# Kernel tuning notes

Hardware: AMD Instinct MI355X
Metric: run time of the kernel (lower is better)

## Reference

```python
import jax, jax.numpy as jnp
import numpy as np

P = 2        # patch_size
HEADS = 1


def _conv(x, w, b, groups=1):
    # NCHW conv, kernel 3x3, SAME padding (stride 1)
    y = jax.lax.conv_general_dilated(
        x, w, window_strides=(1, 1), padding='SAME',
        dimension_numbers=('NCHW', 'OIHW', 'NCHW'),
        feature_group_count=groups)
    return y + b[None, :, None, None]


def _unfold(x, p):
    # torch.nn.Unfold(kernel=p, stride=p): [B,C,h,w] -> [B, C*p*p, n]
    B, C, h, w = x.shape
    x = x.reshape(B, C, h // p, p, w // p, p)
    x = x.transpose(0, 1, 3, 5, 2, 4)  # (B, C, ph, pw, h/p, w/p)
    return x.reshape(B, C * p * p, (h // p) * (w // p))


def _fold(x, p, h, w):
    # inverse of _unfold (non-overlapping patches)
    B = x.shape[0]
    C = x.shape[1] // (p * p)
    x = x.reshape(B, C, p, p, h // p, w // p)
    x = x.transpose(0, 1, 4, 2, 5, 3)  # (B, C, h/p, ph, w/p, pw)
    return x.reshape(B, C, h, w)


def setup_inputs() -> dict:
    key = jax.random.key(0)
    ks = jax.random.split(key, 9)
    c = 64
    x = jax.random.normal(ks[0], (2, 5, c, 64, 64), jnp.float32)
    wq = jax.random.normal(ks[1], (c, 1, 3, 3), jnp.float32) * 0.1
    bq = jax.random.normal(ks[2], (c,), jnp.float32) * 0.1
    wk = jax.random.normal(ks[3], (c, 1, 3, 3), jnp.float32) * 0.1
    bk = jax.random.normal(ks[4], (c,), jnp.float32) * 0.1
    wv = jax.random.normal(ks[5], (c, c, 3, 3), jnp.float32) * 0.05
    bv = jax.random.normal(ks[6], (c,), jnp.float32) * 0.1
    wc = jax.random.normal(ks[7], (c, c, 3, 3), jnp.float32) * 0.05
    bc = jax.random.normal(ks[8], (c,), jnp.float32) * 0.1
    return {"x": x, "wq": wq, "bq": bq, "wk": wk, "bk": bk,
            "wv": wv, "bv": bv, "wc": wc, "bc": bc}


def reference(x, wq, bq, wk, bk, wv, bv, wc, bc):
    b, t, c, h, w = x.shape
    p, H = P, HEADS
    D = p * p * c           # 256
    d = D // H              # per-head dim
    n = (h // p) * (w // p)  # tokens per frame

    xf = x.reshape(b * t, c, h, w)
    q = _conv(xf, wq, bq, groups=c)   # depthwise
    k = _conv(xf, wk, bk, groups=c)   # depthwise
    v = _conv(xf, wv, bv)             # dense conv

    def to_tokens(y):
        # [bt, D, n] -> [b, H, d, t*n]
        u = _unfold(y, p).reshape(b, t, H, d, n)
        return u.transpose(0, 2, 3, 1, 4).reshape(b, H, d, t * n)

    uq, uk, uv = to_tokens(q), to_tokens(k), to_tokens(v)

    attn = jnp.einsum('bhdi,bhdj->bhij', uq, uk) * (d ** -0.5)
    attn = jax.nn.softmax(attn, axis=-1)           # [b,H,tn,tn]
    ax = jnp.einsum('bhij,bhdj->bhid', attn, uv)   # [b,H,tn,d]

    ax = ax.reshape(b, H, t, n, d).transpose(0, 2, 1, 4, 3).reshape(b * t, D, n)
    feat = _fold(ax, p, h, w)                      # [bt, c, h, w]
    out = _conv(feat, wc, bc).reshape(x.shape) + x
    return out
```

## Files before the change

kernel.cpp:

```cpp
#include <hip/hip_runtime.h>
#include <hip/hip_bf16.h>

typedef __attribute__((ext_vector_type(8))) short short8;
typedef __attribute__((ext_vector_type(8))) unsigned short ushort8;
typedef __attribute__((ext_vector_type(4))) unsigned short ushort4v;
typedef __attribute__((ext_vector_type(4))) float f32x4;

#define NTOK 5120
#define DDIM 256

__device__ __forceinline__ unsigned short f2bf(float f) {
  union { float f; unsigned int u; } x; x.f = f;
  unsigned int r = x.u + 0x7FFFu + ((x.u >> 16) & 1u);
  return (unsigned short)(r >> 16);
}

__global__ __launch_bounds__(256) void qk_gen(
    const float* __restrict__ xin, const float* __restrict__ wq,
    const float* __restrict__ bq, const float* __restrict__ wk,
    const float* __restrict__ bk, unsigned short* __restrict__ qt,
    unsigned short* __restrict__ kt)
{
  const int ch = blockIdx.x;
  const int bt = blockIdx.y;
  const int b = bt / 5, tf = bt % 5;
  const int tid = threadIdx.x;
  const float* xp = xin + ((size_t)bt * 64 + ch) * 4096;
  float wqv[9], wkv[9];
  #pragma unroll
  for (int i = 0; i < 9; i++) { wqv[i] = wq[ch * 9 + i]; wkv[i] = wk[ch * 9 + i]; }
  const float bqv = bq[ch], bkv = bk[ch];

  #pragma unroll
  for (int p = 0; p < 4; p++) {
    int pid = tid + p * 256;
    int gy = pid >> 5, gx = pid & 31;
    float v[4][4];
    #pragma unroll
    for (int r = 0; r < 4; r++) {
      int yy = 2 * gy - 1 + r;
      #pragma unroll
      for (int cc = 0; cc < 4; cc++) {
        int xx = 2 * gx - 1 + cc;
        bool ok = (yy >= 0) && (yy < 64) && (xx >= 0) && (xx < 64);
        v[r][cc] = ok ? xp[yy * 64 + xx] : 0.f;
      }
    }
    unsigned short qo[4], ko[4];
    #pragma unroll
    for (int py = 0; py < 2; py++)
      #pragma unroll
      for (int px = 0; px < 2; px++) {
        float aq = bqv, ak = bkv;
        #pragma unroll
        for (int dy = 0; dy < 3; dy++)
          #pragma unroll
          for (int dx = 0; dx < 3; dx++) {
            float xv = v[py + dy][px + dx];
            aq += wqv[dy * 3 + dx] * xv;
            ak += wkv[dy * 3 + dx] * xv;
          }
        qo[py * 2 + px] = f2bf(aq);
        ko[py * 2 + px] = f2bf(ak);
      }
    size_t base = ((size_t)(b * NTOK + tf * 1024 + pid)) * DDIM + ch * 4;
    ushort4v qv = { qo[0], qo[1], qo[2], qo[3] };
    ushort4v kv = { ko[0], ko[1], ko[2], ko[3] };
    *(ushort4v*)(qt + base) = qv;
    *(ushort4v*)(kt + base) = kv;
  }
}

__global__ __launch_bounds__(256) void wt_gen(
    const float* __restrict__ w0, const float* __restrict__ w1,
    unsigned short* __restrict__ o0, unsigned short* __restrict__ o1)
{
  const int tap = blockIdx.x;
  const float* src = blockIdx.y ? w1 : w0;
  unsigned short* dst = blockIdx.y ? o1 : o0;
  const int t = threadIdx.x;
  #pragma unroll
  for (int i = 0; i < 16; i++) {
    int oi = t + i * 256;
    dst[tap * 4096 + oi] = f2bf(src[(size_t)oi * 9 + tap]);
  }
}

__global__ __launch_bounds__(256) void conv_mfma(
    const float* __restrict__ src,
    const unsigned short* __restrict__ wt,
    float* __restrict__ dst)
{
  const int strip = blockIdx.x;
  const int bt = blockIdx.y;
  const int y0 = strip * 4;
  const int tid = threadIdx.x;
  const int sw = tid >> 6, lane = tid & 63;
  const int g = lane >> 4, c = lane & 15;

  __shared__ __align__(16) unsigned short lds_in[6 * 66 * 64];
  __shared__ __align__(16) unsigned short lds_w[64 * 64];

  {
    const int rr0 = lane >> 4;
    const int cb = lane & 15;
    #pragma unroll
    for (int pass = 0; pass < 2; ++pass) {
      int rr = pass * 4 + rr0;
      if (rr < 6) {
        int row = y0 - 1 + rr;
        bool rok = (row >= 0) && (row < 64);
        #pragma unroll 4
        for (int cii = 0; cii < 16; ++cii) {
          int ci = sw * 16 + cii;
          f32x4 v = { 0.f, 0.f, 0.f, 0.f };
          if (rok) v = *(const f32x4*)(src + ((size_t)(bt * 64 + ci)) * 4096 + row * 64 + cb * 4);
          char* base = (char*)lds_in + (rr * 66) * 128 + (ci & 7) * 2;
          #pragma unroll
          for (int q = 0; q < 4; ++q) {
            int lcol = cb * 4 + q + 1;
            *(unsigned short*)(base + lcol * 128 + (((ci >> 3) ^ (lcol & 7)) * 16)) = f2bf(v[q]);
          }
          if (cb == 0)
            *(unsigned short*)(base + (((ci >> 3) ^ 0) * 16)) = 0;
          if (cb == 15)
            *(unsigned short*)(base + 65 * 128 + (((ci >> 3) ^ 1) * 16)) = 0;
        }
      }
    }
  }

  f32x4 acc[4][4];
  #pragma unroll
  for (int ct = 0; ct < 4; ct++)
    #pragma unroll
    for (int xt = 0; xt < 4; xt++) acc[ct][xt] = (f32x4){ 0.f, 0.f, 0.f, 0.f };

  #pragma unroll 1
  for (int tap = 0; tap < 9; ++tap) {
    __syncthreads();
    {
      const unsigned short* wp = wt + tap * 4096;
      #pragma unroll
      for (int h = 0; h < 2; ++h) {
        int el = h * 2048 + tid * 8;
        int co = el >> 6, sl = (el & 63) >> 3;
        short8 wv8 = *(const short8*)(wp + el);
        *(short8*)((char*)lds_w + co * 128 + ((sl ^ (co & 7)) * 16)) = wv8;
      }
    }
    __syncthreads();
    const int dy = tap / 3 - 1, dx = tap % 3 - 1;
    const int rowp = sw + 1 + dy;
    #pragma unroll
    for (int kblk = 0; kblk < 2; ++kblk) {
      short8 af[4], bf[4];
      #pragma unroll
      for (int ct = 0; ct < 4; ++ct)
        af[ct] = *(const short8*)((char*)lds_w + (ct * 16 + c) * 128 + ((((kblk << 2) + g) ^ (c & 7)) * 16));
      #pragma unroll
      for (int xt = 0; xt < 4; ++xt) {
        int lcol = xt * 16 + c + dx + 1;
        bf[xt] = *(const short8*)((char*)lds_in + (rowp * 66 + lcol) * 128 + ((((kblk << 2) + g) ^ (lcol & 7)) * 16));
      }
      #pragma unroll
      for (int ct = 0; ct < 4; ++ct)
        #pragma unroll
        for (int xt = 0; xt < 4; ++xt)
          acc[ct][xt] = __builtin_amdgcn_mfma_f32_16x16x32_bf16(af[ct], bf[xt], acc[ct][xt], 0, 0, 0);
    }
  }

  const int y = y0 + sw;
  float* dp = dst + ((size_t)bt * 64) * 4096 + y * 64;
  #pragma unroll
  for (int ct = 0; ct < 4; ++ct)
    #pragma unroll
    for (int xt = 0; xt < 4; ++xt)
      #pragma unroll
      for (int r = 0; r < 4; ++r) {
        int co = ct * 16 + g * 4 + r;
        dp[(size_t)co * 4096 + xt * 16 + c] = acc[ct][xt][r];
      }
}

__global__ __launch_bounds__(256) void v_combine(
    const float* __restrict__ part, const float* __restrict__ bv,
    unsigned short* __restrict__ vt)
{
  const int co = blockIdx.x;
  const int bt = blockIdx.y;
  const int b = bt / 5, tf = bt % 5;
  const int t = threadIdx.x;
  const int y = t >> 2, xq = (t & 3) * 16;
  const float vb = bv[co];
  const float* p0 = part + ((size_t)bt * 64 + co) * 4096 + y * 64 + xq;
  float val[16];
  #pragma unroll
  for (int q = 0; q < 4; q++) {
    f32x4 a = *(const f32x4*)(p0 + q * 4);
    val[q*4+0] = a[0] + vb; val[q*4+1] = a[1] + vb;
    val[q*4+2] = a[2] + vb; val[q*4+3] = a[3] + vb;
  }
  int py = y & 1, gy = y >> 1;
  ushort8 w0, w1;
  #pragma unroll
  for (int i = 0; i < 8; i++) {
    w0[i] = f2bf(val[2 * i + 0]);
    w1[i] = f2bf(val[2 * i + 1]);
  }
  size_t base0 = ((size_t)(b * DDIM + co * 4 + py * 2)) * NTOK + tf * 1024 + gy * 32 + (xq >> 1);
  *(ushort8*)(vt + base0) = w0;
  *(ushort8*)(vt + base0 + NTOK) = w1;
}

__global__ __launch_bounds__(256) void attn_kernel(
    const unsigned short* __restrict__ qt, const unsigned short* __restrict__ kt,
    const unsigned short* __restrict__ vt, float* __restrict__ po,
    float* __restrict__ pm, float* __restrict__ pl, int jchunk)
{
  const int b = blockIdx.z;
  const int jc = blockIdx.y;
  const int njc = gridDim.y;
  const int i0 = blockIdx.x * 128;
  const int tid = threadIdx.x;
  const int w = tid >> 6, lane = tid & 63;
  const int g = lane >> 4, c = lane & 15;

  __shared__ __align__(16) unsigned short lds_k[64 * 256];
  __shared__ __align__(16) unsigned short lds_v[256 * 64];
  __shared__ __align__(16) unsigned short lds_p[4 * 32 * 64];

  short8 qf[2][8];
  #pragma unroll
  for (int st = 0; st < 2; st++) {
    const unsigned short* qr = qt + ((size_t)(b * NTOK + i0 + w * 32 + st * 16 + c)) * DDIM + g * 8;
    #pragma unroll
    for (int kb = 0; kb < 8; kb++) qf[st][kb] = *(const short8*)(qr + kb * 32);
  }
  f32x4 o[32];
  #pragma unroll
  for (int i = 0; i < 32; i++) o[i] = (f32x4){ 0.f, 0.f, 0.f, 0.f };
  float m[2][4], l[2][4];
  #pragma unroll
  for (int st = 0; st < 2; st++)
    #pragma unroll
    for (int r = 0; r < 4; r++) { m[st][r] = -1e30f; l[st][r] = 0.f; }

  const int sr = tid >> 5, sc = tid & 31;
  const int vdr = tid >> 3, vcc = tid & 7;

  const int jbeg = jc * jchunk;
  for (int j0 = jbeg; j0 < jbeg + jchunk; j0 += 64) {
    #pragma unroll
    for (int p = 0; p < 8; p++) {
      int row = sr + p * 8;
      short8 kv = *(const short8*)(kt + ((size_t)(b * NTOK + j0 + row)) * DDIM + sc * 8);
      *(short8*)((char*)lds_k + row * 512 + ((sc ^ (row & 7)) * 16)) = kv;
    }
    #pragma unroll
    for (int p = 0; p < 8; p++) {
      int dd = vdr + p * 32;
      short8 vv = *(const short8*)(vt + ((size_t)(b * DDIM + dd)) * NTOK + j0 + vcc * 8);
      *(short8*)((char*)lds_v + dd * 128 + ((vcc ^ (dd & 7)) * 16)) = vv;
    }
    __syncthreads();

    f32x4 s0[4], s1[4];
    #pragma unroll
    for (int js = 0; js < 4; js++) {
      s0[js] = (f32x4){ 0.f, 0.f, 0.f, 0.f };
      s1[js] = (f32x4){ 0.f, 0.f, 0.f, 0.f };
      int row = js * 16 + c;
      int sw2 = row & 7;
      #pragma unroll
      for (int kb = 0; kb < 8; kb++) {
        short8 kf = *(const short8*)((char*)lds_k + row * 512 + (((kb * 4 + g) ^ sw2) * 16));
        s0[js] = __builtin_amdgcn_mfma_f32_16x16x32_bf16(qf[0][kb], kf, s0[js], 0, 0, 0);
        s1[js] = __builtin_amdgcn_mfma_f32_16x16x32_bf16(qf[1][kb], kf, s1[js], 0, 0, 0);
      }
    }
    char* pb = (char*)lds_p + w * 4096;
    #pragma unroll
    for (int st = 0; st < 2; st++) {
      float pvv[4][4], alpha[4];
      #pragma unroll
      for (int r = 0; r < 4; r++) {
        float a0 = st ? s1[0][r] : s0[0][r];
        float a1 = st ? s1[1][r] : s0[1][r];
        float a2 = st ? s1[2][r] : s0[2][r];
        float a3 = st ? s1[3][r] : s0[3][r];
        float mx = fmaxf(fmaxf(a0, a1), fmaxf(a2, a3)) * 0.0625f;
        #pragma unroll
        for (int off = 1; off < 16; off <<= 1) mx = fmaxf(mx, __shfl_xor(mx, off));
        float mn = fmaxf(m[st][r], mx);
        alpha[r] = __expf(m[st][r] - mn);
        float p0 = __expf(a0 * 0.0625f - mn);
        float p1 = __expf(a1 * 0.0625f - mn);
        float p2 = __expf(a2 * 0.0625f - mn);
        float p3 = __expf(a3 * 0.0625f - mn);
        pvv[0][r] = p0; pvv[1][r] = p1; pvv[2][r] = p2; pvv[3][r] = p3;
        float sum = p0 + p1 + p2 + p3;
        #pragma unroll
        for (int off = 1; off < 16; off <<= 1) sum += __shfl_xor(sum, off);
        l[st][r] = l[st][r] * alpha[r] + sum;
        m[st][r] = mn;
      }
      f32x4 av = { alpha[0], alpha[1], alpha[2], alpha[3] };
      #pragma unroll
      for (int ds = 0; ds < 16; ds++) o[st * 16 + ds] *= av;
      #pragma unroll
      for (int js = 0; js < 4; js++)
        #pragma unroll
        for (int r = 0; r < 4; r++) {
          int row = st * 16 + 4 * g + r;
          int slot = (js * 2 + (c >> 3)) ^ (row & 7);
          *(unsigned short*)(pb + row * 128 + slot * 16 + (c & 7) * 2) = f2bf(pvv[js][r]);
        }
    }
    short8 pf[2][2];
    #pragma unroll
    for (int st = 0; st < 2; st++)
      #pragma unroll
      for (int k2 = 0; k2 < 2; k2++)
        pf[st][k2] = *(short8*)(pb + (st * 16 + c) * 128 + (((k2 * 4 + g) ^ (c & 7)) * 16));
    #pragma unroll
    for (int ds = 0; ds < 16; ds++) {
      int vrow = ds * 16 + c;
      int sw2 = c & 7;
      #pragma unroll
      for (int k2 = 0; k2 < 2; k2++) {
        short8 vf = *(const short8*)((char*)lds_v + vrow * 128 + (((k2 * 4 + g) ^ sw2) * 16));
        o[ds]      = __builtin_amdgcn_mfma_f32_16x16x32_bf16(pf[0][k2], vf, o[ds], 0, 0, 0);
        o[16 + ds] = __builtin_amdgcn_mfma_f32_16x16x32_bf16(pf[1][k2], vf, o[16 + ds], 0, 0, 0);
      }
    }
    __syncthreads();
  }
  #pragma unroll
  for (int st = 0; st < 2; st++) {
    const size_t rbase = ((size_t)(b * njc + jc)) * NTOK + i0 + w * 32 + st * 16;
    #pragma unroll
    for (int ds = 0; ds < 16; ds++)
      #pragma unroll
      for (int r = 0; r < 4; r++)
        po[(rbase + 4 * g + r) * DDIM + ds * 16 + c] = o[st * 16 + ds][r];
    if (c == 0) {
      #pragma unroll
      for (int r = 0; r < 4; r++) {
        pm[rbase + 4 * g + r] = m[st][r];
        pl[rbase + 4 * g + r] = l[st][r];
      }
    }
  }
}

__global__ __launch_bounds__(256) void attn_combine(
    const float* __restrict__ po, const float* __restrict__ pm,
    const float* __restrict__ pl, float* __restrict__ feat, int njc)
{
  const int b = blockIdx.y;
  const int i0 = blockIdx.x * 64;
  const int t = threadIdx.x;
  const int row = t >> 2, dq = (t & 3) * 64;
  const int i = i0 + row;

  float M = -1e30f, L = 0.f;
  f32x4 acc[16];
  #pragma unroll
  for (int q = 0; q < 16; q++) acc[q] = (f32x4){ 0.f, 0.f, 0.f, 0.f };

  #pragma unroll 1
  for (int jc = 0; jc < njc; jc++) {
    const size_t rb = ((size_t)(b * njc + jc)) * NTOK + i;
    float mj = pm[rb], lj = pl[rb];
    float mn = fmaxf(M, mj);
    float so = __expf(M - mn), sn = __expf(mj - mn);
    const float* pp = po + rb * DDIM + dq;
    #pragma unroll
    for (int q = 0; q < 16; q++) {
      f32x4 v = *(const f32x4*)(pp + q * 4);
      acc[q] = acc[q] * so + v * sn;
    }
    L = L * so + lj * sn;
    M = mn;
  }
  const float inv = 1.f / L;
  const int tf = i >> 10, jn = i & 1023;
  const int gy = jn >> 5, gx = jn & 31;
  const size_t fb = ((size_t)((b * 5 + tf) * 64)) * 4096 + (2 * gy) * 64 + 2 * gx;
  #pragma unroll
  for (int q = 0; q < 16; q++) {
    f32x4 a = acc[q] * inv;
    int ch = (dq + q * 4) >> 2;
    size_t base = fb + (size_t)ch * 4096;
    feat[base] = a[0]; feat[base + 1] = a[1];
    feat[base + 64] = a[2]; feat[base + 65] = a[3];
  }
}

__global__ __launch_bounds__(256) void out_combine(
    const float* __restrict__ part, const float* __restrict__ bc,
    const float* __restrict__ xin, float* __restrict__ out)
{
  const int co = blockIdx.x;
  const int bt = blockIdx.y;
  const int t = threadIdx.x;
  const int y = t >> 2, xq = (t & 3) * 16;
  const float bcv = bc[co];
  const size_t obase = ((size_t)bt * 64 + co) * 4096 + y * 64 + xq;
  const float* p0 = part + obase;
  #pragma unroll
  for (int q = 0; q < 4; q++) {
    f32x4 a = *(const f32x4*)(p0 + q * 4);
    f32x4 xr = *(const f32x4*)(xin + obase + q * 4);
    f32x4 ov;
    ov[0] = a[0] + bcv + xr[0];
    ov[1] = a[1] + bcv + xr[1];
    ov[2] = a[2] + bcv + xr[2];
    ov[3] = a[3] + bcv + xr[3];
    *(f32x4*)(out + obase + q * 4) = ov;
  }
}

extern "C" void kernel_launch(void* const* d_in, const int* in_sizes, int n_in,
                              void* d_out, int out_size, void* d_ws, size_t ws_size,
                              hipStream_t stream) {
  const float* x  = (const float*)d_in[0];
  const float* wq = (const float*)d_in[1];
  const float* bq = (const float*)d_in[2];
  const float* wk = (const float*)d_in[3];
  const float* bk = (const float*)d_in[4];
  const float* wv = (const float*)d_in[5];
  const float* bv = (const float*)d_in[6];
  const float* wc = (const float*)d_in[7];
  const float* bc = (const float*)d_in[8];
  float* out = (float*)d_out;

  char* ws = (char*)d_ws;
  unsigned short* qt = (unsigned short*)(ws);
  unsigned short* kt = (unsigned short*)(ws + 5242880);
  unsigned short* vt = (unsigned short*)(ws + 10485760);
  float*          ft = (float*)(ws + 15728640);
  unsigned short* wtv = (unsigned short*)(ws + 26214400);
  unsigned short* wtc = (unsigned short*)(ws + 26288128);
  const size_t big_off = 26361856;
  float*          big = (float*)(ws + big_off);

  int njc = 10;
  size_t po_bytes = (size_t)2 * njc * NTOK * DDIM * 4;
  if (big_off + po_bytes + 2 * (size_t)2 * njc * NTOK * 4 > ws_size) {
    njc = 4;
    po_bytes = (size_t)2 * njc * NTOK * DDIM * 4;
  }
  float* pm = (float*)(ws + big_off + po_bytes);
  float* pl = pm + (size_t)2 * njc * NTOK;
  const int jchunk = NTOK / njc;

  wt_gen      <<<dim3(9, 2), 256, 0, stream>>>(wv, wc, wtv, wtc);
  qk_gen      <<<dim3(64, 10), 256, 0, stream>>>(x, wq, bq, wk, bk, qt, kt);
  conv_mfma   <<<dim3(16, 10), 256, 0, stream>>>(x, wtv, big);
  v_combine   <<<dim3(64, 10), 256, 0, stream>>>(big, bv, vt);
  attn_kernel <<<dim3(40, njc, 2), 256, 0, stream>>>(qt, kt, vt, big, pm, pl, jchunk);
  attn_combine<<<dim3(80, 2), 256, 0, stream>>>(big, pm, pl, ft, njc);
  conv_mfma   <<<dim3(16, 10), 256, 0, stream>>>(ft, wtc, big);
  out_combine <<<dim3(64, 10), 256, 0, stream>>>(big, bc, x, out);
}
```

Measured before the change: 295.4 us.

## Fuse conv epilogues, halve conv strips, store bf16 partials, raise split count

The bias-add and v-token scatter are folded into the first conv's epilogue, and the bias-plus-residual into the second conv's, which removes two separate kernels and their fp32 round trips. Conv blocks now cover 2 rows each (4 waves split over rows and channel halves), giving 320 blocks instead of 160. Attention partial outputs are stored as bf16, the P staging buffer now reuses lds_k to cut LDS use, launch bounds request 2 blocks per CU, and the j-split count rises to 20 when workspace allows. The trade-offs are bf16 rounding on the partial outputs, scattered 2-byte global stores in the v epilogue, and a reuse of the lds_k region that depends on correct barrier placement.

After: 365.2 us. 1.24x slower.

```diff
diff --git a/kernel.cpp b/kernel.cpp
--- a/kernel.cpp
+++ b/kernel.cpp
@@ -13,6 +13,9 @@
   union { float f; unsigned int u; } x; x.f = f;
   unsigned int r = x.u + 0x7FFFu + ((x.u >> 16) & 1u);
   return (unsigned short)(r >> 16);
+}
+__device__ __forceinline__ float bf2f(unsigned short u) {
+  union { unsigned int i; float f; } x; x.i = ((unsigned int)u) << 16; return x.f;
 }
 
 __global__ __launch_bounds__(256) void qk_gen(
@@ -86,53 +89,52 @@
   }
 }
 
+template<int MODE>
 __global__ __launch_bounds__(256) void conv_mfma(
-    const float* __restrict__ src,
-    const unsigned short* __restrict__ wt,
-    float* __restrict__ dst)
+    const float* __restrict__ src, const unsigned short* __restrict__ wt,
+    const float* __restrict__ bias, const float* __restrict__ resid,
+    float* __restrict__ dstf, unsigned short* __restrict__ vt)
 {
   const int strip = blockIdx.x;
   const int bt = blockIdx.y;
-  const int y0 = strip * 4;
+  const int y0 = strip * 2;
   const int tid = threadIdx.x;
   const int sw = tid >> 6, lane = tid & 63;
+  const int ry = sw >> 1, ch = sw & 1;
   const int g = lane >> 4, c = lane & 15;
 
-  __shared__ __align__(16) unsigned short lds_in[6 * 66 * 64];
+  __shared__ __align__(16) unsigned short lds_in[4 * 66 * 64];
   __shared__ __align__(16) unsigned short lds_w[64 * 64];
 
   {
-    const int rr0 = lane >> 4;
+    const int rr = lane >> 4;
     const int cb = lane & 15;
-    #pragma unroll
-    for (int pass = 0; pass < 2; ++pass) {
-      int rr = pass * 4 + rr0;
-      if (rr < 6) {
-        int row = y0 - 1 + rr;
-        bool rok = (row >= 0) && (row < 64);
-        #pragma unroll 4
-        for (int cii = 0; cii < 16; ++cii) {
-          int ci = sw * 16 + cii;
-          f32x4 v = { 0.f, 0.f, 0.f, 0.f };
-          if (rok) v = *(const f32x4*)(src + ((size_t)(bt * 64 + ci)) * 4096 + row * 64 + cb * 4);
-          char* base = (char*)lds_in + (rr * 66) * 128 + (ci & 7) * 2;
-          #pragma unroll
-          for (int q = 0; q < 4; ++q) {
-            int lcol = cb * 4 + q + 1;
-            *(unsigned short*)(base + lcol * 128 + (((ci >> 3) ^ (lcol & 7)) * 16)) = f2bf(v[q]);
-          }
-          if (cb == 0)
-            *(unsigned short*)(base + (((ci >> 3) ^ 0) * 16)) = 0;
-          if (cb == 15)
-            *(unsigned short*)(base + 65 * 128 + (((ci >> 3) ^ 1) * 16)) = 0;
-        }
-      }
-    }
-  }
-
-  f32x4 acc[4][4];
-  #pragma unroll
-  for (int ct = 0; ct < 4; ct++)
+    const int row = y0 - 1 + rr;
+    const bool rok = (row >= 0) && (row < 64);
+    #pragma unroll
+    for (int pp = 0; pp < 8; ++pp) {
+      const int ci0 = sw * 16 + pp * 2;
+      f32x4 va = { 0.f, 0.f, 0.f, 0.f }, vb = { 0.f, 0.f, 0.f, 0.f };
+      if (rok) {
+        va = *(const f32x4*)(src + ((size_t)(bt * 64 + ci0)) * 4096 + row * 64 + cb * 4);
+        vb = *(const f32x4*)(src + ((size_t)(bt * 64 + ci0 + 1)) * 4096 + row * 64 + cb * 4);
+      }
+      char* rbase = (char*)lds_in + (rr * 66) * 128 + (ci0 & 7) * 2;
+      const int sl = ci0 >> 3;
+      #pragma unroll
+      for (int q = 0; q < 4; ++q) {
+        int lcol = cb * 4 + q + 1;
+        unsigned int pk = (unsigned int)f2bf(va[q]) | ((unsigned int)f2bf(vb[q]) << 16);
+        *(unsigned int*)(rbase + lcol * 128 + ((sl ^ (lcol & 7)) * 16)) = pk;
+      }
+      if (cb == 0)  *(unsigned int*)(rbase + ((sl ^ 0) * 16)) = 0u;
+      if (cb == 15) *(unsigned int*)(rbase + 65 * 128 + ((sl ^ 1) * 16)) = 0u;
+    }
+  }
+
+  f32x4 acc[2][4];
+  #pragma unroll
+  for (int ct = 0; ct < 2; ct++)
     #pragma unroll
     for (int xt = 0; xt < 4; xt++) acc[ct][xt] = (f32x4){ 0.f, 0.f, 0.f, 0.f };
 
@@ -151,72 +153,66 @@
     }
     __syncthreads();
     const int dy = tap / 3 - 1, dx = tap % 3 - 1;
-    const int rowp = sw + 1 + dy;
+    const int rowp = ry + 1 + dy;
     #pragma unroll
     for (int kblk = 0; kblk < 2; ++kblk) {
-      short8 af[4], bf[4];
-      #pragma unroll
-      for (int ct = 0; ct < 4; ++ct)
-        af[ct] = *(const short8*)((char*)lds_w + (ct * 16 + c) * 128 + ((((kblk << 2) + g) ^ (c & 7)) * 16));
+      short8 af[2], bf[4];
+      #pragma unroll
+      for (int ct = 0; ct < 2; ++ct) {
+        int co = ch * 32 + ct * 16 + c;
+        af[ct] = *(const short8*)((char*)lds_w + co * 128 + (((kblk * 4 + g) ^ (co & 7)) * 16));
+      }
       #pragma unroll
       for (int xt = 0; xt < 4; ++xt) {
         int lcol = xt * 16 + c + dx + 1;
-        bf[xt] = *(const short8*)((char*)lds_in + (rowp * 66 + lcol) * 128 + ((((kblk << 2) + g) ^ (lcol & 7)) * 16));
-      }
-      #pragma unroll
-      for (int ct = 0; ct < 4; ++ct)
+        bf[xt] = *(const short8*)((char*)lds_in + (rowp * 66 + lcol) * 128 + (((kblk * 4 + g) ^ (lcol & 7)) * 16));
+      }
+      #pragma unroll
+      for (int ct = 0; ct < 2; ++ct)
         #pragma unroll
         for (int xt = 0; xt < 4; ++xt)
           acc[ct][xt] = __builtin_amdgcn_mfma_f32_16x16x32_bf16(af[ct], bf[xt], acc[ct][xt], 0, 0, 0);
     }
   }
 
-  const int y = y0 + sw;
-  float* dp = dst + ((size_t)bt * 64) * 4096 + y * 64;
-  #pragma unroll
-  for (int ct = 0; ct < 4; ++ct)
-    #pragma unroll
-    for (int xt = 0; xt < 4; ++xt)
+  const int y = y0 + ry;
+  if (MODE == 0) {
+    const int b = bt / 5, tf = bt % 5;
+    const int py = y & 1, gy = y >> 1;
+    #pragma unroll
+    for (int ct = 0; ct < 2; ++ct)
       #pragma unroll
       for (int r = 0; r < 4; ++r) {
-        int co = ct * 16 + g * 4 + r;
-        dp[(size_t)co * 4096 + xt * 16 + c] = acc[ct][xt][r];
-      }
-}
-
-__global__ __launch_bounds__(256) void v_combine(
-    const float* __restrict__ part, const float* __restrict__ bv,
-    unsigned short* __restrict__ vt)
-{
-  const int co = blockIdx.x;
-  const int bt = blockIdx.y;
-  const int b = bt / 5, tf = bt % 5;
-  const int t = threadIdx.x;
-  const int y = t >> 2, xq = (t & 3) * 16;
-  const float vb = bv[co];
-  const float* p0 = part + ((size_t)bt * 64 + co) * 4096 + y * 64 + xq;
-  float val[16];
-  #pragma unroll
-  for (int q = 0; q < 4; q++) {
-    f32x4 a = *(const f32x4*)(p0 + q * 4);
-    val[q*4+0] = a[0] + vb; val[q*4+1] = a[1] + vb;
-    val[q*4+2] = a[2] + vb; val[q*4+3] = a[3] + vb;
-  }
-  int py = y & 1, gy = y >> 1;
-  ushort8 w0, w1;
-  #pragma unroll
-  for (int i = 0; i < 8; i++) {
-    w0[i] = f2bf(val[2 * i + 0]);
-    w1[i] = f2bf(val[2 * i + 1]);
-  }
-  size_t base0 = ((size_t)(b * DDIM + co * 4 + py * 2)) * NTOK + tf * 1024 + gy * 32 + (xq >> 1);
-  *(ushort8*)(vt + base0) = w0;
-  *(ushort8*)(vt + base0 + NTOK) = w1;
-}
-
-__global__ __launch_bounds__(256) void attn_kernel(
+        const int co = ch * 32 + ct * 16 + g * 4 + r;
+        const float bv = bias[co];
+        #pragma unroll
+        for (int xt = 0; xt < 4; ++xt) {
+          int x = xt * 16 + c;
+          int d = co * 4 + py * 2 + (x & 1);
+          int tok = tf * 1024 + gy * 32 + (x >> 1);
+          vt[((size_t)(b * DDIM + d)) * NTOK + tok] = f2bf(acc[ct][xt][r] + bv);
+        }
+      }
+  } else {
+    #pragma unroll
+    for (int ct = 0; ct < 2; ++ct)
+      #pragma unroll
+      for (int r = 0; r < 4; ++r) {
+        const int co = ch * 32 + ct * 16 + g * 4 + r;
+        const float bv = bias[co];
+        const size_t rowb = ((size_t)(bt * 64 + co)) * 4096 + (size_t)y * 64;
+        #pragma unroll
+        for (int xt = 0; xt < 4; ++xt) {
+          int x = xt * 16 + c;
+          dstf[rowb + x] = acc[ct][xt][r] + bv + resid[rowb + x];
+        }
+      }
+  }
+}
+
+__global__ __launch_bounds__(256, 2) void attn_kernel(
     const unsigned short* __restrict__ qt, const unsigned short* __restrict__ kt,
-    const unsigned short* __restrict__ vt, float* __restrict__ po,
+    const unsigned short* __restrict__ vt, unsigned short* __restrict__ po,
     float* __restrict__ pm, float* __restrict__ pl, int jchunk)
 {
   const int b = blockIdx.z;
@@ -229,7 +225,6 @@
 
   __shared__ __align__(16) unsigned short lds_k[64 * 256];
   __shared__ __align__(16) unsigned short lds_v[256 * 64];
-  __shared__ __align__(16) unsigned short lds_p[4 * 32 * 64];
 
   short8 qf[2][8];
   #pragma unroll
@@ -249,6 +244,7 @@
 
   const int sr = tid >> 5, sc = tid & 31;
   const int vdr = tid >> 3, vcc = tid & 7;
+  char* pb = (char*)lds_k + w * 4096;
 
   const int jbeg = jc * jchunk;
   for (int j0 = jbeg; j0 < jbeg + jchunk; j0 += 64) {
@@ -280,44 +276,70 @@
         s1[js] = __builtin_amdgcn_mfma_f32_16x16x32_bf16(qf[1][kb], kf, s1[js], 0, 0, 0);
       }
     }
-    char* pb = (char*)lds_p + w * 4096;
-    #pragma unroll
-    for (int st = 0; st < 2; st++) {
-      float pvv[4][4], alpha[4];
+    float pvv[4][4], alpha[4];
+    #pragma unroll
+    for (int r = 0; r < 4; r++) {
+      float mx = fmaxf(fmaxf(s0[0][r], s0[1][r]), fmaxf(s0[2][r], s0[3][r])) * 0.0625f;
+      #pragma unroll
+      for (int off = 1; off < 16; off <<= 1) mx = fmaxf(mx, __shfl_xor(mx, off));
+      float mn = fmaxf(m[0][r], mx);
+      alpha[r] = __expf(m[0][r] - mn);
+      float p0 = __expf(s0[0][r] * 0.0625f - mn);
+      float p1 = __expf(s0[1][r] * 0.0625f - mn);
+      float p2 = __expf(s0[2][r] * 0.0625f - mn);
+      float p3 = __expf(s0[3][r] * 0.0625f - mn);
+      pvv[0][r] = p0; pvv[1][r] = p1; pvv[2][r] = p2; pvv[3][r] = p3;
+      float sum = p0 + p1 + p2 + p3;
+      #pragma unroll
+      for (int off = 1; off < 16; off <<= 1) sum += __shfl_xor(sum, off);
+      l[0][r] = l[0][r] * alpha[r] + sum;
+      m[0][r] = mn;
+    }
+    {
+      f32x4 av = { alpha[0], alpha[1], alpha[2], alpha[3] };
+      #pragma unroll
+      for (int ds = 0; ds < 16; ds++) o[ds] *= av;
+    }
+    __syncthreads();
+    #pragma unroll
+    for (int js = 0; js < 4; js++)
       #pragma unroll
       for (int r = 0; r < 4; r++) {
-        float a0 = st ? s1[0][r] : s0[0][r];
-        float a1 = st ? s1[1][r] : s0[1][r];
-        float a2 = st ? s1[2][r] : s0[2][r];
-        float a3 = st ? s1[3][r] : s0[3][r];
-        float mx = fmaxf(fmaxf(a0, a1), fmaxf(a2, a3)) * 0.0625f;
-        #pragma unroll
-        for (int off = 1; off < 16; off <<= 1) mx = fmaxf(mx, __shfl_xor(mx, off));
-        float mn = fmaxf(m[st][r], mx);
-        alpha[r] = __expf(m[st][r] - mn);
-        float p0 = __expf(a0 * 0.0625f - mn);
-        float p1 = __expf(a1 * 0.0625f - mn);
-        float p2 = __expf(a2 * 0.0625f - mn);
-        float p3 = __expf(a3 * 0.0625f - mn);
-        pvv[0][r] = p0; pvv[1][r] = p1; pvv[2][r] = p2; pvv[3][r] = p3;
-        float sum = p0 + p1 + p2 + p3;
-        #pragma unroll
-        for (int off = 1; off < 16; off <<= 1) sum += __shfl_xor(sum, off);
-        l[st][r] = l[st][r] * alpha[r] + sum;
-        m[st][r] = mn;
-      }
+        int row = 4 * g + r;
+        int slot = (js * 2 + (c >> 3)) ^ (row & 7);
+        *(unsigned short*)(pb + row * 128 + slot * 16 + (c & 7) * 2) = f2bf(pvv[js][r]);
+      }
+    #pragma unroll
+    for (int r = 0; r < 4; r++) {
+      float mx = fmaxf(fmaxf(s1[0][r], s1[1][r]), fmaxf(s1[2][r], s1[3][r])) * 0.0625f;
+      #pragma unroll
+      for (int off = 1; off < 16; off <<= 1) mx = fmaxf(mx, __shfl_xor(mx, off));
+      float mn = fmaxf(m[1][r], mx);
+      alpha[r] = __expf(m[1][r] - mn);
+      float p0 = __expf(s1[0][r] * 0.0625f - mn);
+      float p1 = __expf(s1[1][r] * 0.0625f - mn);
+      float p2 = __expf(s1[2][r] * 0.0625f - mn);
+      float p3 = __expf(s1[3][r] * 0.0625f - mn);
+      pvv[0][r] = p0; pvv[1][r] = p1; pvv[2][r] = p2; pvv[3][r] = p3;
+      float sum = p0 + p1 + p2 + p3;
+      #pragma unroll
+      for (int off = 1; off < 16; off <<= 1) sum += __shfl_xor(sum, off);
+      l[1][r] = l[1][r] * alpha[r] + sum;
+      m[1][r] = mn;
+    }
+    {
       f32x4 av = { alpha[0], alpha[1], alpha[2], alpha[3] };
       #pragma unroll
-      for (int ds = 0; ds < 16; ds++) o[st * 16 + ds] *= av;
-      #pragma unroll
-      for (int js = 0; js < 4; js++)
-        #pragma unroll
-        for (int r = 0; r < 4; r++) {
-          int row = st * 16 + 4 * g + r;
-          int slot = (js * 2 + (c >> 3)) ^ (row & 7);
-          *(unsigned short*)(pb + row * 128 + slot * 16 + (c & 7) * 2) = f2bf(pvv[js][r]);
-        }
-    }
+      for (int ds = 0; ds < 16; ds++) o[16 + ds] *= av;
+    }
+    #pragma unroll
+    for (int js = 0; js < 4; js++)
+      #pragma unroll
+      for (int r = 0; r < 4; r++) {
+        int row = 16 + 4 * g + r;
+        int slot = (js * 2 + (c >> 3)) ^ (row & 7);
+        *(unsigned short*)(pb + row * 128 + slot * 16 + (c & 7) * 2) = f2bf(pvv[js][r]);
+      }
     short8 pf[2][2];
     #pragma unroll
     for (int st = 0; st < 2; st++)
@@ -344,7 +366,7 @@
     for (int ds = 0; ds < 16; ds++)
       #pragma unroll
       for (int r = 0; r < 4; r++)
-        po[(rbase + 4 * g + r) * DDIM + ds * 16 + c] = o[st * 16 + ds][r];
+        po[(rbase + 4 * g + r) * DDIM + ds * 16 + c] = f2bf(o[st * 16 + ds][r]);
     if (c == 0) {
       #pragma unroll
       for (int r = 0; r < 4; r++) {
@@ -356,7 +378,7 @@
 }
 
 __global__ __launch_bounds__(256) void attn_combine(
-    const float* __restrict__ po, const float* __restrict__ pm,
+    const unsigned short* __restrict__ po, const float* __restrict__ pm,
     const float* __restrict__ pl, float* __restrict__ feat, int njc)
 {
   const int b = blockIdx.y;
@@ -366,9 +388,9 @@
   const int i = i0 + row;
 
   float M = -1e30f, L = 0.f;
-  f32x4 acc[16];
-  #pragma unroll
-  for (int q = 0; q < 16; q++) acc[q] = (f32x4){ 0.f, 0.f, 0.f, 0.f };
+  float acc[64];
+  #pragma unroll
+  for (int q = 0; q < 64; q++) acc[q] = 0.f;
 
   #pragma unroll 1
   for (int jc = 0; jc < njc; jc++) {
@@ -376,11 +398,13 @@
     float mj = pm[rb], lj = pl[rb];
     float mn = fmaxf(M, mj);
     float so = __expf(M - mn), sn = __expf(mj - mn);
-    const float* pp = po + rb * DDIM + dq;
-    #pragma unroll
-    for (int q = 0; q < 16; q++) {
-      f32x4 v = *(const f32x4*)(pp + q * 4);
-      acc[q] = acc[q] * so + v * sn;
+    const unsigned short* pp = po + rb * DDIM + dq;
+    #pragma unroll
+    for (int q8 = 0; q8 < 8; q8++) {
+      ushort8 uu = *(const ushort8*)(pp + q8 * 8);
+      #pragma unroll
+      for (int e = 0; e < 8; e++)
+        acc[q8 * 8 + e] = acc[q8 * 8 + e] * so + bf2f(uu[e]) * sn;
     }
     L = L * so + lj * sn;
     M = mn;
@@ -391,35 +415,12 @@
   const size_t fb = ((size_t)((b * 5 + tf) * 64)) * 4096 + (2 * gy) * 64 + 2 * gx;
   #pragma unroll
   for (int q = 0; q < 16; q++) {
-    f32x4 a = acc[q] * inv;
     int ch = (dq + q * 4) >> 2;
     size_t base = fb + (size_t)ch * 4096;
-    feat[base] = a[0]; feat[base + 1] = a[1];
-    feat[base + 64] = a[2]; feat[base + 65] = a[3];
-  }
-}
-
-__global__ __launch_bounds__(256) void out_combine(
-    const float* __restrict__ part, const float* __restrict__ bc,
-    const float* __restrict__ xin, float* __restrict__ out)
-{
-  const int co = blockIdx.x;
-  const int bt = blockIdx.y;
-  const int t = threadIdx.x;
-  const int y = t >> 2, xq = (t & 3) * 16;
-  const float bcv = bc[co];
-  const size_t obase = ((size_t)bt * 64 + co) * 4096 + y * 64 + xq;
-  const float* p0 = part + obase;
-  #pragma unroll
-  for (int q = 0; q < 4; q++) {
-    f32x4 a = *(const f32x4*)(p0 + q * 4);
-    f32x4 xr = *(const f32x4*)(xin + obase + q * 4);
-    f32x4 ov;
-    ov[0] = a[0] + bcv + xr[0];
-    ov[1] = a[1] + bcv + xr[1];
-    ov[2] = a[2] + bcv + xr[2];
-    ov[3] = a[3] + bcv + xr[3];
-    *(f32x4*)(out + obase + q * 4) = ov;
+    feat[base]      = acc[q * 4 + 0] * inv;
+    feat[base + 1]  = acc[q * 4 + 1] * inv;
+    feat[base + 64] = acc[q * 4 + 2] * inv;
+    feat[base + 65] = acc[q * 4 + 3] * inv;
   }
 }
 
@@ -445,24 +446,23 @@
   unsigned short* wtv = (unsigned short*)(ws + 26214400);
   unsigned short* wtc = (unsigned short*)(ws + 26288128);
   const size_t big_off = 26361856;
-  float*          big = (float*)(ws + big_off);
-
-  int njc = 10;
-  size_t po_bytes = (size_t)2 * njc * NTOK * DDIM * 4;
-  if (big_off + po_bytes + 2 * (size_t)2 * njc * NTOK * 4 > ws_size) {
-    njc = 4;
-    po_bytes = (size_t)2 * njc * NTOK * DDIM * 4;
+  unsigned short* po = (unsigned short*)(ws + big_off);
+
+  int njc = 20;
+  size_t po_bytes = (size_t)2 * njc * NTOK * DDIM * 2;
+  while (njc > 4 &&
+         big_off + po_bytes + (size_t)4 * 2 * njc * NTOK * 2 > ws_size) {
+    njc = (njc == 20) ? 10 : 4;
+    po_bytes = (size_t)2 * njc * NTOK * DDIM * 2;
   }
   float* pm = (float*)(ws + big_off + po_bytes);
   float* pl = pm + (size_t)2 * njc * NTOK;
   const int jchunk = NTOK / njc;
 
-  wt_gen      <<<dim3(9, 2), 256, 0, stream>>>(wv, wc, wtv, wtc);
-  qk_gen      <<<dim3(64, 10), 256, 0, stream>>>(x, wq, bq, wk, bk, qt, kt);
-  conv_mfma   <<<dim3(16, 10), 256, 0, stream>>>(x, wtv, big);
-  v_combine   <<<dim3(64, 10), 256, 0, stream>>>(big, bv, vt);
-  attn_kernel <<<dim3(40, njc, 2), 256, 0, stream>>>(qt, kt, vt, big, pm, pl, jchunk);
-  attn_combine<<<dim3(80, 2), 256, 0, stream>>>(big, pm, pl, ft, njc);
-  conv_mfma   <<<dim3(16, 10), 256, 0, stream>>>(ft, wtc, big);
-  out_combine <<<dim3(64, 10), 256, 0, stream>>>(big, bc, x, out);
-}
+  wt_gen        <<<dim3(9, 2), 256, 0, stream>>>(wv, wc, wtv, wtc);
+  qk_gen        <<<dim3(64, 10), 256, 0, stream>>>(x, wq, bq, wk, bk, qt, kt);
+  conv_mfma<0>  <<<dim3(32, 10), 256, 0, stream>>>(x, wtv, bv, nullptr, nullptr, vt);
+  attn_kernel   <<<dim3(40, njc, 2), 256, 0, stream>>>(qt, kt, vt, po, pm, pl, jchunk);
+  attn_combine  <<<dim3(80, 2), 256, 0, stream>>>(po, pm, pl, ft, njc);
+  conv_mfma<1>  <<<dim3(32, 10), 256, 0, stream>>>(ft, wtc, bc, x, out, nullptr);
+}
```
